# Performance work log

Hardware: AMD Instinct MI355X
Metric: run time of the kernel (lower is better)

Reference implementation:

```python
import jax, jax.numpy as jnp
import numpy as np

N_NODES = 10000
N_EDGES = 160000
D = 512
DROPOUT_P = 0.5
NEG_SLOPE = 0.25


def setup_inputs() -> dict:
    key = jax.random.key(0)
    ks = jax.random.split(key, 8)
    H = jax.random.normal(ks[0], (N_NODES, D), dtype=jnp.float32)
    rows = jax.random.randint(ks[1], (N_EDGES,), 0, N_NODES)
    cols = jax.random.randint(ks[2], (N_EDGES,), 0, N_NODES)
    vals = jax.random.uniform(ks[3], (N_EDGES,), dtype=jnp.float32)
    # xavier-normal-ish weights, zero bias (matches torch init)
    std = float(np.sqrt(2.0 / (D + D)))
    W1 = jax.random.normal(ks[4], (D, D), dtype=jnp.float32) * std
    b1 = jnp.zeros((D,), dtype=jnp.float32)
    W2 = jax.random.normal(ks[5], (D, D), dtype=jnp.float32) * std
    b2 = jnp.zeros((D,), dtype=jnp.float32)
    return {"H": H, "rows": rows, "cols": cols, "vals": vals,
            "W1": W1, "b1": b1, "W2": W2, "b2": b2}


def _spmm(rows, cols, vals, dense):
    # sparse [N,N] @ dense [N,D] via gather + segment-sum
    gathered = vals[:, None] * dense[cols]          # [E, D]
    return jax.ops.segment_sum(gathered, rows, num_segments=N_NODES)


def _leaky_relu(x):
    return jnp.where(x >= 0, x, NEG_SLOPE * x)


def reference(H, rows, cols, vals, W1, b1, W2, b2):
    # layer 1: dense GEMM -> SpMM -> bias -> leaky_relu -> dropout(training=True)
    h = _spmm(rows, cols, vals, H @ W1) + b1
    h = _leaky_relu(h)
    keep = jax.random.bernoulli(jax.random.key(42), 1.0 - DROPOUT_P, h.shape)
    h = jnp.where(keep, h / (1.0 - DROPOUT_P), 0.0)
    # layer 2
    h = _spmm(rows, cols, vals, h @ W2) + b2
    return _leaky_relu(h)
```

## Files before the change

kernel.cpp:

```cpp
#include <hip/hip_runtime.h>
#include <stdint.h>

#define N_NODES 10000
#define M_PAD   10112
#define N_EDGES 160000
#define DIM     512
#define N_ELEMS 5120000
#define NEG_SLOPE 0.25f
#define ELL_W   64

typedef short          short8   __attribute__((ext_vector_type(8)));
typedef unsigned short ushort8v __attribute__((ext_vector_type(8)));
typedef __bf16         bf16x8   __attribute__((ext_vector_type(8)));
typedef float          f32x4    __attribute__((ext_vector_type(4)));

__device__ __forceinline__ unsigned short f2bf(float f) {
    uint32_t u = __builtin_bit_cast(uint32_t, f);
    uint32_t r = (u + 0x7fffu + ((u >> 16) & 1u)) >> 16;
    return (unsigned short)r;
}
__device__ __forceinline__ float b2f(unsigned short u) {
    return __builtin_bit_cast(float, (uint32_t)u << 16);
}

__device__ __forceinline__ uint32_t rotl32(uint32_t x, uint32_t d) {
    return (x << d) | (x >> (32u - d));
}
__device__ __forceinline__ void threefry_42(uint32_t x0, uint32_t x1,
                                            uint32_t& o0, uint32_t& o1) {
    const uint32_t ks0 = 0u, ks1 = 42u, ks2 = 0x1BD11BDAu ^ 42u;
    x0 += ks0; x1 += ks1;
#define TF_R4(a,b,c,d) \
    x0 += x1; x1 = rotl32(x1,a); x1 ^= x0; \
    x0 += x1; x1 = rotl32(x1,b); x1 ^= x0; \
    x0 += x1; x1 = rotl32(x1,c); x1 ^= x0; \
    x0 += x1; x1 = rotl32(x1,d); x1 ^= x0;
    TF_R4(13,15,26,6);  x0 += ks1; x1 += ks2 + 1u;
    TF_R4(17,29,16,24); x0 += ks2; x1 += ks0 + 2u;
    TF_R4(13,15,26,6);  x0 += ks0; x1 += ks1 + 3u;
    TF_R4(17,29,16,24); x0 += ks1; x1 += ks2 + 4u;
    TF_R4(13,15,26,6);  x0 += ks2; x1 += ks0 + 5u;
#undef TF_R4
    o0 = x0; o1 = x1;
}

#define CONV_BLKS 5000
#define TR_BLKS   64
#define EZ_BLKS   1250
#define ZERO_BLKS 10

__device__ __forceinline__ void transpose_tile(const float* __restrict__ W,
                                               unsigned short* __restrict__ WT,
                                               int tile, float (*ts)[65]) {
    int k0 = (tile & 7) * 64, n0 = (tile >> 3) * 64;
    int tx = threadIdx.x & 15, ty = threadIdx.x >> 4;
    #pragma unroll
    for (int i = 0; i < 4; ++i) {
        int k = i * 16 + ty;
        float4 v = *(const float4*)&W[(size_t)(k0 + k) * DIM + n0 + tx * 4];
        ts[k][tx * 4 + 0] = v.x; ts[k][tx * 4 + 1] = v.y;
        ts[k][tx * 4 + 2] = v.z; ts[k][tx * 4 + 3] = v.w;
    }
    __syncthreads();
    #pragma unroll
    for (int i = 0; i < 4; ++i) {
        int n = i * 16 + ty;
        ushort4 o;
        o.x = f2bf(ts[tx * 4 + 0][n]); o.y = f2bf(ts[tx * 4 + 1][n]);
        o.z = f2bf(ts[tx * 4 + 2][n]); o.w = f2bf(ts[tx * 4 + 3][n]);
        *(ushort4*)&WT[(size_t)(n0 + n) * DIM + k0 + tx * 4] = o;
    }
}

__global__ __launch_bounds__(256)
void prep_kernel(const float* __restrict__ H, const float* __restrict__ W1,
                 const float* __restrict__ W2, unsigned short* __restrict__ Abf,
                 unsigned short* __restrict__ WT1, unsigned short* __restrict__ WT2,
                 int4* __restrict__ epack4, int* __restrict__ deg) {
    __shared__ float ts[64][65];
    int b = blockIdx.x;
    if (b < CONV_BLKS) {
        int i = b * 256 + threadIdx.x;
        float4 v = ((const float4*)H)[i];
        ushort4 o;
        o.x = f2bf(v.x); o.y = f2bf(v.y); o.z = f2bf(v.z); o.w = f2bf(v.w);
        ((ushort4*)Abf)[i] = o;
    } else if (b < CONV_BLKS + TR_BLKS) {
        transpose_tile(W1, WT1, b - CONV_BLKS, ts);
    } else if (b < CONV_BLKS + 2 * TR_BLKS) {
        transpose_tile(W2, WT2, b - CONV_BLKS - TR_BLKS, ts);
    } else if (b < CONV_BLKS + 2 * TR_BLKS + EZ_BLKS) {
        int i = (b - CONV_BLKS - 2 * TR_BLKS) * 256 + threadIdx.x;
        epack4[i] = make_int4(0, 0, 0, 0);
    } else {
        int i = (b - CONV_BLKS - 2 * TR_BLKS - EZ_BLKS) * 1024 + threadIdx.x * 4;
        #pragma unroll
        for (int j = 0; j < 4; ++j)
            if (i + j < N_NODES) deg[i + j] = 0;
    }
}

__global__ void ell_scatter(const int* __restrict__ rows, const int* __restrict__ cols,
                            const float* __restrict__ vals, int* __restrict__ deg,
                            int2* __restrict__ epack) {
    int e = blockIdx.x * blockDim.x + threadIdx.x;
    if (e < N_EDGES) {
        int r = rows[e];
        int p = atomicAdd(&deg[r], 1);
        epack[(size_t)r * ELL_W + p] = make_int2(cols[e], __float_as_int(vals[e]));
    }
}

__global__ __launch_bounds__(256)
void mfma_gemm(const unsigned short* __restrict__ A, const unsigned short* __restrict__ BT,
               unsigned short* __restrict__ C, int M) {
    __shared__ short8 As[1024];
    __shared__ short8 Bs[1024];
    int tid  = threadIdx.x;
    int wid  = tid >> 6, lane = tid & 63;
    int bm   = blockIdx.x * 128;
    int bn   = blockIdx.y * 128;
    int wm   = (wid >> 1) * 64, wn = (wid & 1) * 64;

    f32x4 acc[4][4] = {};
    int srow = lane >> 3;
    int sslot = lane & 7;

    for (int k0 = 0; k0 < DIM; k0 += 64) {
        #pragma unroll
        for (int c = 0; c < 4; ++c) {
            int chunk = wid * 4 + c;
            int r  = chunk * 8 + srow;
            int ks = sslot ^ (r & 7);
            const unsigned short* ga = A  + (size_t)(bm + r) * DIM + k0 + ks * 8;
            const unsigned short* gb = BT + (size_t)(bn + r) * DIM + k0 + ks * 8;
            __builtin_amdgcn_global_load_lds(
                (const __attribute__((address_space(1))) void*)ga,
                (__attribute__((address_space(3))) void*)&As[chunk * 64], 16, 0, 0);
            __builtin_amdgcn_global_load_lds(
                (const __attribute__((address_space(1))) void*)gb,
                (__attribute__((address_space(3))) void*)&Bs[chunk * 64], 16, 0, 0);
        }
        __syncthreads();

        int lrow = lane & 15;
        int kgrp = lane >> 4;
        #pragma unroll
        for (int ks = 0; ks < 2; ++ks) {
            short8 af[4], bfr[4];
            #pragma unroll
            for (int i = 0; i < 4; ++i) {
                int r = wm + i * 16 + lrow;
                af[i]  = As[r * 8 + ((ks * 4 + kgrp) ^ (r & 7))];
                int n = wn + i * 16 + lrow;
                bfr[i] = Bs[n * 8 + ((ks * 4 + kgrp) ^ (n & 7))];
            }
            #pragma unroll
            for (int i = 0; i < 4; ++i)
                #pragma unroll
                for (int j = 0; j < 4; ++j)
                    acc[i][j] = __builtin_amdgcn_mfma_f32_16x16x32_bf16(
                        __builtin_bit_cast(bf16x8, af[i]),
                        __builtin_bit_cast(bf16x8, bfr[j]), acc[i][j], 0, 0, 0);
        }
        __syncthreads();
    }

    int crow = (lane >> 4) * 4;
    int ccol = lane & 15;
    #pragma unroll
    for (int i = 0; i < 4; ++i) {
        #pragma unroll
        for (int r = 0; r < 4; ++r) {
            int row = bm + wm + i * 16 + crow + r;
            if (row < M) {
                size_t base = (size_t)row * DIM + bn + wn + ccol;
                #pragma unroll
                for (int j = 0; j < 4; ++j)
                    C[base + j * 16] = f2bf(acc[i][j][r]);
            }
        }
    }
}

template <int LAYER>
__global__ __launch_bounds__(256)
void spmm_kernel(const unsigned short* __restrict__ X, const int* __restrict__ deg,
                 const int2* __restrict__ epack, const float* __restrict__ bias,
                 void* __restrict__ outp) {
    int row  = blockIdx.x * 4 + (threadIdx.x >> 6);
    int lane = threadIdx.x & 63;
    int d  = deg[row];
    int dp = (d + 7) & ~7;
    const int2* ep = epack + (size_t)row * ELL_W;
    const ushort8v* X8 = (const ushort8v*)X;

    float acc[8] = {};
    int base = 0;
    for (; base + 16 <= dp; base += 16) {
        int4 eA = *(const int4*)(ep + base);
        int4 eB = *(const int4*)(ep + base + 2);
        int4 eC = *(const int4*)(ep + base + 4);
        int4 eD = *(const int4*)(ep + base + 6);
        int4 eE = *(const int4*)(ep + base + 8);
        int4 eF = *(const int4*)(ep + base + 10);
        int4 eG = *(const int4*)(ep + base + 12);
        int4 eH = *(const int4*)(ep + base + 14);
        ushort8v x0 = X8[(size_t)eA.x * 64 + lane];
        ushort8v x1 = X8[(size_t)eA.z * 64 + lane];
        ushort8v x2 = X8[(size_t)eB.x * 64 + lane];
        ushort8v x3 = X8[(size_t)eB.z * 64 + lane];
        ushort8v x4 = X8[(size_t)eC.x * 64 + lane];
        ushort8v x5 = X8[(size_t)eC.z * 64 + lane];
        ushort8v x6 = X8[(size_t)eD.x * 64 + lane];
        ushort8v x7 = X8[(size_t)eD.z * 64 + lane];
        ushort8v x8 = X8[(size_t)eE.x * 64 + lane];
        ushort8v x9 = X8[(size_t)eE.z * 64 + lane];
        ushort8v xa = X8[(size_t)eF.x * 64 + lane];
        ushort8v xb = X8[(size_t)eF.z * 64 + lane];
        ushort8v xc = X8[(size_t)eG.x * 64 + lane];
        ushort8v xd = X8[(size_t)eG.z * 64 + lane];
        ushort8v xe = X8[(size_t)eH.x * 64 + lane];
        ushort8v xf = X8[(size_t)eH.z * 64 + lane];
        float v0 = __int_as_float(eA.y), v1 = __int_as_float(eA.w);
        float v2 = __int_as_float(eB.y), v3 = __int_as_float(eB.w);
        float v4 = __int_as_float(eC.y), v5 = __int_as_float(eC.w);
        float v6 = __int_as_float(eD.y), v7 = __int_as_float(eD.w);
        float v8 = __int_as_float(eE.y), v9 = __int_as_float(eE.w);
        float va = __int_as_float(eF.y), vb = __int_as_float(eF.w);
        float vc = __int_as_float(eG.y), vd = __int_as_float(eG.w);
        float ve = __int_as_float(eH.y), vf = __int_as_float(eH.w);
        #pragma unroll
        for (int j = 0; j < 8; ++j) {
            acc[j] = fmaf(v0, b2f(x0[j]), acc[j]);
            acc[j] = fmaf(v1, b2f(x1[j]), acc[j]);
            acc[j] = fmaf(v2, b2f(x2[j]), acc[j]);
            acc[j] = fmaf(v3, b2f(x3[j]), acc[j]);
            acc[j] = fmaf(v4, b2f(x4[j]), acc[j]);
            acc[j] = fmaf(v5, b2f(x5[j]), acc[j]);
            acc[j] = fmaf(v6, b2f(x6[j]), acc[j]);
            acc[j] = fmaf(v7, b2f(x7[j]), acc[j]);
            acc[j] = fmaf(v8, b2f(x8[j]), acc[j]);
            acc[j] = fmaf(v9, b2f(x9[j]), acc[j]);
            acc[j] = fmaf(va, b2f(xa[j]), acc[j]);
            acc[j] = fmaf(vb, b2f(xb[j]), acc[j]);
            acc[j] = fmaf(vc, b2f(xc[j]), acc[j]);
            acc[j] = fmaf(vd, b2f(xd[j]), acc[j]);
            acc[j] = fmaf(ve, b2f(xe[j]), acc[j]);
            acc[j] = fmaf(vf, b2f(xf[j]), acc[j]);
        }
    }
    if (base < dp) {
        int4 eA = *(const int4*)(ep + base);
        int4 eB = *(const int4*)(ep + base + 2);
        int4 eC = *(const int4*)(ep + base + 4);
        int4 eD = *(const int4*)(ep + base + 6);
        ushort8v x0 = X8[(size_t)eA.x * 64 + lane];
        ushort8v x1 = X8[(size_t)eA.z * 64 + lane];
        ushort8v x2 = X8[(size_t)eB.x * 64 + lane];
        ushort8v x3 = X8[(size_t)eB.z * 64 + lane];
        ushort8v x4 = X8[(size_t)eC.x * 64 + lane];
        ushort8v x5 = X8[(size_t)eC.z * 64 + lane];
        ushort8v x6 = X8[(size_t)eD.x * 64 + lane];
        ushort8v x7 = X8[(size_t)eD.z * 64 + lane];
        float v0 = __int_as_float(eA.y), v1 = __int_as_float(eA.w);
        float v2 = __int_as_float(eB.y), v3 = __int_as_float(eB.w);
        float v4 = __int_as_float(eC.y), v5 = __int_as_float(eC.w);
        float v6 = __int_as_float(eD.y), v7 = __int_as_float(eD.w);
        #pragma unroll
        for (int j = 0; j < 8; ++j) {
            acc[j] = fmaf(v0, b2f(x0[j]), acc[j]);
            acc[j] = fmaf(v1, b2f(x1[j]), acc[j]);
            acc[j] = fmaf(v2, b2f(x2[j]), acc[j]);
            acc[j] = fmaf(v3, b2f(x3[j]), acc[j]);
            acc[j] = fmaf(v4, b2f(x4[j]), acc[j]);
            acc[j] = fmaf(v5, b2f(x5[j]), acc[j]);
            acc[j] = fmaf(v6, b2f(x6[j]), acc[j]);
            acc[j] = fmaf(v7, b2f(x7[j]), acc[j]);
        }
    }

    float4 bi0 = ((const float4*)bias)[lane * 2];
    float4 bi1 = ((const float4*)bias)[lane * 2 + 1];
    float bb[8] = { bi0.x, bi0.y, bi0.z, bi0.w, bi1.x, bi1.y, bi1.z, bi1.w };
    float r[8];
    #pragma unroll
    for (int j = 0; j < 8; ++j) {
        float v = acc[j] + bb[j];
        r[j] = (v >= 0.f) ? v : NEG_SLOPE * v;
    }
    if (LAYER == 1) {
        uint32_t e0 = (uint32_t)row * DIM + lane * 8;
        ushort8v o;
        #pragma unroll
        for (int j = 0; j < 8; ++j) {
            uint32_t o0, o1;
            threefry_42(0u, e0 + j, o0, o1);
            uint32_t bits = o0 ^ o1;
            float v = ((int)bits >= 0) ? r[j] * 2.0f : 0.0f;
            o[j] = f2bf(v);
        }
        ((ushort8v*)outp)[(size_t)row * 64 + lane] = o;
    } else {
        float4 o0 = make_float4(r[0], r[1], r[2], r[3]);
        float4 o1 = make_float4(r[4], r[5], r[6], r[7]);
        ((float4*)outp)[(size_t)row * 128 + lane * 2]     = o0;
        ((float4*)outp)[(size_t)row * 128 + lane * 2 + 1] = o1;
    }
}

extern "C" void kernel_launch(void* const* d_in, const int* in_sizes, int n_in,
                              void* d_out, int out_size, void* d_ws, size_t ws_size,
                              hipStream_t stream) {
    const float* H    = (const float*)d_in[0];
    const int*   rows = (const int*)  d_in[1];
    const int*   cols = (const int*)  d_in[2];
    const float* vals = (const float*)d_in[3];
    const float* W1   = (const float*)d_in[4];
    const float* b1   = (const float*)d_in[5];
    const float* W2   = (const float*)d_in[6];
    const float* b2   = (const float*)d_in[7];
    float* out = (float*)d_out;

    char* ws = (char*)d_ws;
    size_t off = 0;
    auto alloc = [&](size_t bytes) -> void* {
        off = (off + 255) & ~(size_t)255;
        void* p = ws + off;
        off += bytes;
        return p;
    };
    int*  deg   = (int*) alloc((size_t)N_NODES * 4);
    int2* epack = (int2*)alloc((size_t)N_NODES * ELL_W * 8);
    unsigned short* WT1 = (unsigned short*)alloc((size_t)DIM * DIM * 2);
    unsigned short* WT2 = (unsigned short*)alloc((size_t)DIM * DIM * 2);
    unsigned short* Abf = (unsigned short*)alloc((size_t)M_PAD * DIM * 2);
    unsigned short* hbf = (unsigned short*)alloc((size_t)M_PAD * DIM * 2);
    unsigned short* Xbf = (unsigned short*)alloc((size_t)N_NODES * DIM * 2);

    int prep_blocks = CONV_BLKS + 2 * TR_BLKS + EZ_BLKS + ZERO_BLKS;
    prep_kernel<<<prep_blocks, 256, 0, stream>>>(H, W1, W2, Abf, WT1, WT2,
                                                 (int4*)epack, deg);
    ell_scatter<<<(N_EDGES + 255) / 256, 256, 0, stream>>>(rows, cols, vals, deg, epack);

    dim3 ggrid(M_PAD / 128, DIM / 128);
    mfma_gemm<<<ggrid, 256, 0, stream>>>(Abf, WT1, Xbf, N_NODES);
    spmm_kernel<1><<<N_NODES / 4, 256, 0, stream>>>(Xbf, deg, epack, b1, hbf);
    mfma_gemm<<<ggrid, 256, 0, stream>>>(hbf, WT2, Xbf, N_NODES);
    spmm_kernel<2><<<N_NODES / 4, 256, 0, stream>>>(Xbf, deg, epack, b2, out);
}
```

Baseline: 102.2 us.

## Split SpMM row across four column-quarter blocks with edge-parallel lane groups

The SpMM kernel now gives each wavefront one quarter (128 columns) of a row and splits its 64 lanes into four edge groups of 16 lanes, which reduce their partial sums with cross-lane shuffles. The grid grows fourfold, and block indices are swizzled so the quarter-blocks of the same rows run close together. The goal is more parallelism and memory-level concurrency per row, with fewer dependent FMAs per lane. The cost is more blocks, repeated reads of the edge lists and degree for each quarter, shuffle reductions, and three quarters of the lanes sitting idle during the epilogue.

```diff
diff --git a/kernel.cpp b/kernel.cpp
--- a/kernel.cpp
+++ b/kernel.cpp
@@ -188,124 +188,88 @@
 void spmm_kernel(const unsigned short* __restrict__ X, const int* __restrict__ deg,
                  const int2* __restrict__ epack, const float* __restrict__ bias,
                  void* __restrict__ outp) {
-    int row  = blockIdx.x * 4 + (threadIdx.x >> 6);
+    int b    = blockIdx.x;
+    int q    = (b & 7) >> 1;
+    int pi   = ((b >> 3) << 1) | (b & 1);
+    int row  = pi * 4 + (threadIdx.x >> 6);
     int lane = threadIdx.x & 63;
+    int eg   = lane >> 4;
+    int li   = lane & 15;
     int d  = deg[row];
     int dp = (d + 7) & ~7;
     const int2* ep = epack + (size_t)row * ELL_W;
     const ushort8v* X8 = (const ushort8v*)X;
+    size_t qoff = (size_t)q * 16 + li;
 
     float acc[8] = {};
     int base = 0;
     for (; base + 16 <= dp; base += 16) {
-        int4 eA = *(const int4*)(ep + base);
-        int4 eB = *(const int4*)(ep + base + 2);
-        int4 eC = *(const int4*)(ep + base + 4);
-        int4 eD = *(const int4*)(ep + base + 6);
-        int4 eE = *(const int4*)(ep + base + 8);
-        int4 eF = *(const int4*)(ep + base + 10);
-        int4 eG = *(const int4*)(ep + base + 12);
-        int4 eH = *(const int4*)(ep + base + 14);
-        ushort8v x0 = X8[(size_t)eA.x * 64 + lane];
-        ushort8v x1 = X8[(size_t)eA.z * 64 + lane];
-        ushort8v x2 = X8[(size_t)eB.x * 64 + lane];
-        ushort8v x3 = X8[(size_t)eB.z * 64 + lane];
-        ushort8v x4 = X8[(size_t)eC.x * 64 + lane];
-        ushort8v x5 = X8[(size_t)eC.z * 64 + lane];
-        ushort8v x6 = X8[(size_t)eD.x * 64 + lane];
-        ushort8v x7 = X8[(size_t)eD.z * 64 + lane];
-        ushort8v x8 = X8[(size_t)eE.x * 64 + lane];
-        ushort8v x9 = X8[(size_t)eE.z * 64 + lane];
-        ushort8v xa = X8[(size_t)eF.x * 64 + lane];
-        ushort8v xb = X8[(size_t)eF.z * 64 + lane];
-        ushort8v xc = X8[(size_t)eG.x * 64 + lane];
-        ushort8v xd = X8[(size_t)eG.z * 64 + lane];
-        ushort8v xe = X8[(size_t)eH.x * 64 + lane];
-        ushort8v xf = X8[(size_t)eH.z * 64 + lane];
-        float v0 = __int_as_float(eA.y), v1 = __int_as_float(eA.w);
-        float v2 = __int_as_float(eB.y), v3 = __int_as_float(eB.w);
-        float v4 = __int_as_float(eC.y), v5 = __int_as_float(eC.w);
-        float v6 = __int_as_float(eD.y), v7 = __int_as_float(eD.w);
-        float v8 = __int_as_float(eE.y), v9 = __int_as_float(eE.w);
-        float va = __int_as_float(eF.y), vb = __int_as_float(eF.w);
-        float vc = __int_as_float(eG.y), vd = __int_as_float(eG.w);
-        float ve = __int_as_float(eH.y), vf = __int_as_float(eH.w);
+        int2 eA = ep[base      + eg];
+        int2 eB = ep[base + 4  + eg];
+        int2 eC = ep[base + 8  + eg];
+        int2 eD = ep[base + 12 + eg];
+        ushort8v xA = X8[(size_t)eA.x * 64 + qoff];
+        ushort8v xB = X8[(size_t)eB.x * 64 + qoff];
+        ushort8v xC = X8[(size_t)eC.x * 64 + qoff];
+        ushort8v xD = X8[(size_t)eD.x * 64 + qoff];
+        float vA = __int_as_float(eA.y), vB = __int_as_float(eB.y);
+        float vC = __int_as_float(eC.y), vD = __int_as_float(eD.y);
         #pragma unroll
         for (int j = 0; j < 8; ++j) {
-            acc[j] = fmaf(v0, b2f(x0[j]), acc[j]);
-            acc[j] = fmaf(v1, b2f(x1[j]), acc[j]);
-            acc[j] = fmaf(v2, b2f(x2[j]), acc[j]);
-            acc[j] = fmaf(v3, b2f(x3[j]), acc[j]);
-            acc[j] = fmaf(v4, b2f(x4[j]), acc[j]);
-            acc[j] = fmaf(v5, b2f(x5[j]), acc[j]);
-            acc[j] = fmaf(v6, b2f(x6[j]), acc[j]);
-            acc[j] = fmaf(v7, b2f(x7[j]), acc[j]);
-            acc[j] = fmaf(v8, b2f(x8[j]), acc[j]);
-            acc[j] = fmaf(v9, b2f(x9[j]), acc[j]);
-            acc[j] = fmaf(va, b2f(xa[j]), acc[j]);
-            acc[j] = fmaf(vb, b2f(xb[j]), acc[j]);
-            acc[j] = fmaf(vc, b2f(xc[j]), acc[j]);
-            acc[j] = fmaf(vd, b2f(xd[j]), acc[j]);
-            acc[j] = fmaf(ve, b2f(xe[j]), acc[j]);
-            acc[j] = fmaf(vf, b2f(xf[j]), acc[j]);
+            acc[j] = fmaf(vA, b2f(xA[j]), acc[j]);
+            acc[j] = fmaf(vB, b2f(xB[j]), acc[j]);
+            acc[j] = fmaf(vC, b2f(xC[j]), acc[j]);
+            acc[j] = fmaf(vD, b2f(xD[j]), acc[j]);
         }
     }
     if (base < dp) {
-        int4 eA = *(const int4*)(ep + base);
-        int4 eB = *(const int4*)(ep + base + 2);
-        int4 eC = *(const int4*)(ep + base + 4);
-        int4 eD = *(const int4*)(ep + base + 6);
-        ushort8v x0 = X8[(size_t)eA.x * 64 + lane];
-        ushort8v x1 = X8[(size_t)eA.z * 64 + lane];
-        ushort8v x2 = X8[(size_t)eB.x * 64 + lane];
-        ushort8v x3 = X8[(size_t)eB.z * 64 + lane];
-        ushort8v x4 = X8[(size_t)eC.x * 64 + lane];
-        ushort8v x5 = X8[(size_t)eC.z * 64 + lane];
-        ushort8v x6 = X8[(size_t)eD.x * 64 + lane];
-        ushort8v x7 = X8[(size_t)eD.z * 64 + lane];
-        float v0 = __int_as_float(eA.y), v1 = __int_as_float(eA.w);
-        float v2 = __int_as_float(eB.y), v3 = __int_as_float(eB.w);
-        float v4 = __int_as_float(eC.y), v5 = __int_as_float(eC.w);
-        float v6 = __int_as_float(eD.y), v7 = __int_as_float(eD.w);
+        int2 eA = ep[base     + eg];
+        int2 eB = ep[base + 4 + eg];
+        ushort8v xA = X8[(size_t)eA.x * 64 + qoff];
+        ushort8v xB = X8[(size_t)eB.x * 64 + qoff];
+        float vA = __int_as_float(eA.y), vB = __int_as_float(eB.y);
         #pragma unroll
         for (int j = 0; j < 8; ++j) {
-            acc[j] = fmaf(v0, b2f(x0[j]), acc[j]);
-            acc[j] = fmaf(v1, b2f(x1[j]), acc[j]);
-            acc[j] = fmaf(v2, b2f(x2[j]), acc[j]);
-            acc[j] = fmaf(v3, b2f(x3[j]), acc[j]);
-            acc[j] = fmaf(v4, b2f(x4[j]), acc[j]);
-            acc[j] = fmaf(v5, b2f(x5[j]), acc[j]);
-            acc[j] = fmaf(v6, b2f(x6[j]), acc[j]);
-            acc[j] = fmaf(v7, b2f(x7[j]), acc[j]);
-        }
-    }
-
-    float4 bi0 = ((const float4*)bias)[lane * 2];
-    float4 bi1 = ((const float4*)bias)[lane * 2 + 1];
-    float bb[8] = { bi0.x, bi0.y, bi0.z, bi0.w, bi1.x, bi1.y, bi1.z, bi1.w };
-    float r[8];
+            acc[j] = fmaf(vA, b2f(xA[j]), acc[j]);
+            acc[j] = fmaf(vB, b2f(xB[j]), acc[j]);
+        }
+    }
+
     #pragma unroll
     for (int j = 0; j < 8; ++j) {
-        float v = acc[j] + bb[j];
-        r[j] = (v >= 0.f) ? v : NEG_SLOPE * v;
-    }
-    if (LAYER == 1) {
-        uint32_t e0 = (uint32_t)row * DIM + lane * 8;
-        ushort8v o;
+        acc[j] += __shfl_xor(acc[j], 16, 64);
+        acc[j] += __shfl_xor(acc[j], 32, 64);
+    }
+
+    if (eg == 0) {
+        int c0 = q * 128 + li * 8;
+        float4 bi0 = *(const float4*)&bias[c0];
+        float4 bi1 = *(const float4*)&bias[c0 + 4];
+        float bb[8] = { bi0.x, bi0.y, bi0.z, bi0.w, bi1.x, bi1.y, bi1.z, bi1.w };
+        float r[8];
         #pragma unroll
         for (int j = 0; j < 8; ++j) {
-            uint32_t o0, o1;
-            threefry_42(0u, e0 + j, o0, o1);
-            uint32_t bits = o0 ^ o1;
-            float v = ((int)bits >= 0) ? r[j] * 2.0f : 0.0f;
-            o[j] = f2bf(v);
-        }
-        ((ushort8v*)outp)[(size_t)row * 64 + lane] = o;
-    } else {
-        float4 o0 = make_float4(r[0], r[1], r[2], r[3]);
-        float4 o1 = make_float4(r[4], r[5], r[6], r[7]);
-        ((float4*)outp)[(size_t)row * 128 + lane * 2]     = o0;
-        ((float4*)outp)[(size_t)row * 128 + lane * 2 + 1] = o1;
+            float v = acc[j] + bb[j];
+            r[j] = (v >= 0.f) ? v : NEG_SLOPE * v;
+        }
+        if (LAYER == 1) {
+            uint32_t e0 = (uint32_t)row * DIM + c0;
+            ushort8v o;
+            #pragma unroll
+            for (int j = 0; j < 8; ++j) {
+                uint32_t o0, o1;
+                threefry_42(0u, e0 + j, o0, o1);
+                uint32_t bits = o0 ^ o1;
+                float v = ((int)bits >= 0) ? r[j] * 2.0f : 0.0f;
+                o[j] = f2bf(v);
+            }
+            ((ushort8v*)outp)[(size_t)row * 64 + q * 16 + li] = o;
+        } else {
+            float4 o0 = make_float4(r[0], r[1], r[2], r[3]);
+            float4 o1 = make_float4(r[4], r[5], r[6], r[7]);
+            ((float4*)outp)[(size_t)row * 128 + q * 32 + li * 2]     = o0;
+            ((float4*)outp)[(size_t)row * 128 + q * 32 + li * 2 + 1] = o1;
+        }
     }
 }
 
@@ -345,7 +309,7 @@
 
     dim3 ggrid(M_PAD / 128, DIM / 128);
     mfma_gemm<<<ggrid, 256, 0, stream>>>(Abf, WT1, Xbf, N_NODES);
-    spmm_kernel<1><<<N_NODES / 4, 256, 0, stream>>>(Xbf, deg, epack, b1, hbf);
+    spmm_kernel<1><<<N_NODES, 256, 0, stream>>>(Xbf, deg, epack, b1, hbf);
     mfma_gemm<<<ggrid, 256, 0, stream>>>(hbf, WT2, Xbf, N_NODES);
-    spmm_kernel<2><<<N_NODES / 4, 256, 0, stream>>>(Xbf, deg, epack, b2, out);
-}
+    spmm_kernel<2><<<N_NODES, 256, 0, stream>>>(Xbf, deg, epack, b2, out);
+}
```

Measured after the change: 125.8 us. 23.1% more time.
